# Optimization experiments

Hardware: AMD Instinct MI355X
Metric: run time of the kernel (lower is better)

The kernel has to match this reference:

```python
import jax, jax.numpy as jnp
import numpy as np

B, S, HID = 2, 2048, 1024
H, D = 16, 64
SCALE = D ** -0.5


def setup_inputs() -> dict:
    key = jax.random.key(0)
    ks = jax.random.split(key, 7)
    std = HID ** -0.5
    return {
        "x": jax.random.normal(ks[0], (B, S, HID), jnp.float32),
        "Wq": jax.random.normal(ks[1], (HID, HID), jnp.float32) * std,
        "Wk": jax.random.normal(ks[2], (HID, HID), jnp.float32) * std,
        "Wv": jax.random.normal(ks[3], (HID, HID), jnp.float32) * std,
        "Wf": jax.random.normal(ks[4], (H, HID), jnp.float32) * std,
        "bf": jnp.zeros((H,), jnp.float32),
        "Wo": jax.random.normal(ks[5], (HID, HID), jnp.float32) * std,
    }


def reference(x, Wq, Wk, Wv, Wf, bf, Wo):
    b, s, _ = x.shape
    # projections (torch Linear: y = x @ W.T), reshape to [b, h, s, d]
    q = (x @ Wq.T).reshape(b, s, H, D).transpose(0, 2, 1, 3)
    k = (x @ Wk.T).reshape(b, s, H, D).transpose(0, 2, 1, 3)
    v = (x @ Wv.T).reshape(b, s, H, D).transpose(0, 2, 1, 3)
    # forget gate: [b, h, s]
    f = jax.nn.sigmoid(x @ Wf.T + bf).transpose(0, 2, 1)
    cum_log_f = jnp.cumsum(jnp.log(f + 1e-6), axis=-1)  # [b, h, s]
    # bias[i, j] = cum[i] - cum[j]
    bias = cum_log_f[..., :, None] - cum_log_f[..., None, :]  # [b, h, s, s]
    causal = jnp.tril(jnp.ones((s, s), bool))
    bias = jnp.where(causal, bias, -jnp.inf)
    scores = jnp.einsum("bhid,bhjd->bhij", q, k) * SCALE + bias
    attn = jax.nn.softmax(scores, axis=-1)
    out = jnp.einsum("bhij,bhjd->bhid", attn, v)  # [b, h, s, d]
    out = out.transpose(0, 2, 1, 3).reshape(b, s, H * D)
    return out @ Wo.T
```

## Files before the change

kernel.cpp:

```cpp
#include <hip/hip_runtime.h>
#include <hip/hip_bf16.h>
#include <math.h>

typedef __attribute__((ext_vector_type(8))) short bf16x8;
typedef __attribute__((ext_vector_type(4))) short s16x4;
typedef __attribute__((ext_vector_type(4))) float f32x4;
typedef __attribute__((ext_vector_type(2))) int i32x2;

constexpr int NB = 2, NS = 2048, NHID = 1024, NH = 16, ND = 64;
constexpr float FSCALE = 0.125f;
constexpr float LOG2E  = 1.44269504088896f;
constexpr int QBLK = 128, NT = NS / QBLK;
constexpr float DROP_MARGIN = 30.0f;

__device__ __forceinline__ short f2bf(float f) {
    union { __hip_bfloat16 h; short s; } u;
    u.h = __float2bfloat16(f);
    return u.s;
}

__device__ __forceinline__ float bf2f(short s) {
    union { unsigned u; float f; } u;
    u.u = ((unsigned)(unsigned short)s) << 16;
    return u.f;
}

__device__ __forceinline__ void gload16(const void* g, void* l) {
    __builtin_amdgcn_global_load_lds(
        (const __attribute__((address_space(1))) unsigned*)g,
        (__attribute__((address_space(3))) unsigned*)l, 16, 0, 0);
}

__device__ __forceinline__ unsigned lds_addr(void* p) {
    return (unsigned)(size_t)(__attribute__((address_space(3))) void*)p;
}

__global__ __launch_bounds__(256)
void cast_kernel(const float* __restrict__ x,
                 const float* __restrict__ Wq, const float* __restrict__ Wk,
                 const float* __restrict__ Wv, const float* __restrict__ Wo,
                 short* __restrict__ xb,
                 short* __restrict__ Wqb, short* __restrict__ Wkb,
                 short* __restrict__ Wvb, short* __restrict__ Wob) {
    const int bx = blockIdx.x;
    const float* s; short* d; size_t i;
    if (bx < 2048) {
        s = x; d = xb;
        i = ((size_t)bx*256 + threadIdx.x)*8;
    } else {
        const int widx = (bx - 2048) >> 9, blk = (bx - 2048) & 511;
        switch (widx) {
            case 0:  s = Wq; d = Wqb; break;
            case 1:  s = Wk; d = Wkb; break;
            case 2:  s = Wv; d = Wvb; break;
            default: s = Wo; d = Wob; break;
        }
        i = ((size_t)blk*256 + threadIdx.x)*8;
    }
    float4 a = *(const float4*)(s+i);
    float4 b = *(const float4*)(s+i+4);
    bf16x8 o;
    o[0]=f2bf(a.x); o[1]=f2bf(a.y); o[2]=f2bf(a.z); o[3]=f2bf(a.w);
    o[4]=f2bf(b.x); o[5]=f2bf(b.y); o[6]=f2bf(b.z); o[7]=f2bf(b.w);
    *(bf16x8*)(d+i) = o;
}

__global__ __launch_bounds__(256)
void fgate_kernel(const float* __restrict__ X, const float* __restrict__ Wf,
                  const float* __restrict__ bfb, float* __restrict__ LF) {
    const int lane = threadIdx.x & 63, w = threadIdx.x >> 6;
    const int m = blockIdx.x;
    const int b = m >> 11, s = m & (NS - 1);
    float xv[16];
    #pragma unroll
    for (int c = 0; c < 16; ++c) xv[c] = X[(size_t)m * NHID + c * 64 + lane];
    #pragma unroll
    for (int hh = 0; hh < 4; ++hh) {
        const int h = w * 4 + hh;
        float p = 0.f;
        #pragma unroll
        for (int c = 0; c < 16; ++c)
            p = fmaf(xv[c], Wf[(size_t)h * NHID + c * 64 + lane], p);
        #pragma unroll
        for (int off = 32; off > 0; off >>= 1) p += __shfl_down(p, off);
        if (lane == 0) {
            float z = p + bfb[h];
            float f = 1.f / (1.f + expf(-z));
            LF[(size_t)(b * NH + h) * NS + s] = __log2f(f + 1e-6f);
        }
    }
}

template<int FM, int FN, int MODE>
__device__ __forceinline__ void gemm_body(
    const short* __restrict__ A, const short* __restrict__ Bm,
    float* __restrict__ Cf, short* __restrict__ Cb,
    int N, int K, float mult, int bx, int by, short* As, short* Bs)
{
    constexpr int BM = FM*32, BN = FN*32;
    const int t = threadIdx.x, w = t>>6, l = t&63, g = l>>4, r = l&15;
    const int m0 = by*BM, n0 = bx*BN;
    const int wr = (w>>1)*(FM*16), wc = (w&1)*(FN*16);
    f32x4 acc[FM][FN] = {};
    for (int k0 = 0; k0 < K; k0 += 32) {
        #pragma unroll
        for (int c = 0; c < (BM*4)/256; ++c) {
            int ci = (c*4 + w)*64 + l;
            gload16(A + (size_t)(m0 + (ci>>2))*K + k0 + (ci&3)*8, As + (c*4+w)*512);
        }
        #pragma unroll
        for (int c = 0; c < (BN*4)/256; ++c) {
            int ci = (c*4 + w)*64 + l;
            gload16(Bm + (size_t)(n0 + (ci>>2))*K + k0 + (ci&3)*8, Bs + (c*4+w)*512);
        }
        __syncthreads();
        bf16x8 af[FM], bfv[FN];
        #pragma unroll
        for (int fm = 0; fm < FM; ++fm)
            af[fm] = *(const bf16x8*)(As + (wr + fm*16 + r)*32 + g*8);
        #pragma unroll
        for (int fn = 0; fn < FN; ++fn)
            bfv[fn] = *(const bf16x8*)(Bs + (wc + fn*16 + r)*32 + g*8);
        #pragma unroll
        for (int fm = 0; fm < FM; ++fm)
            #pragma unroll
            for (int fn = 0; fn < FN; ++fn)
                acc[fm][fn] = __builtin_amdgcn_mfma_f32_16x16x32_bf16(
                    af[fm], bfv[fn], acc[fm][fn], 0, 0, 0);
        __syncthreads();
    }
    #pragma unroll
    for (int fm = 0; fm < FM; ++fm)
        #pragma unroll
        for (int fn = 0; fn < FN; ++fn)
            #pragma unroll
            for (int rr = 0; rr < 4; ++rr) {
                int m = m0 + wr + fm*16 + g*4 + rr;
                int n = n0 + wc + fn*16 + r;
                float v = acc[fm][fn][rr] * mult;
                if (MODE == 0) {
                    Cf[(size_t)m*N + n] = v;
                } else {
                    int b = m >> 11, s = m & (NS-1), hh = n >> 6, d = n & (ND-1);
                    Cb[((size_t)(b*NH + hh)*NS + s)*ND + d] = f2bf(v);
                }
            }
}

__global__ __launch_bounds__(256)
void gemm_qkv_kernel(const short* __restrict__ X,
                     const short* __restrict__ Wq, const short* __restrict__ Wk,
                     const short* __restrict__ Wv,
                     short* __restrict__ Q, short* __restrict__ Kd, short* __restrict__ V)
{
    __shared__ short As[128*32], Bs[128*32];
    const int fl = blockIdx.x + 8*blockIdx.y + 256*blockIdx.z;
    const int wk = (fl & 7)*96 + (fl >> 3);
    const int bx = wk & 7, by = (wk >> 3) & 31, bz = wk >> 8;
    const short* Bm; short* Dst; float mult;
    if (bz == 0)      { Bm = Wq; Dst = Q;  mult = FSCALE * LOG2E; }
    else if (bz == 1) { Bm = Wk; Dst = Kd; mult = 1.f; }
    else              { Bm = Wv; Dst = V;  mult = 1.f; }
    gemm_body<4,4,1>(X, Bm, nullptr, Dst, NHID, NHID, mult, bx, by, As, Bs);
}

__global__ __launch_bounds__(256)
void gemm_out_kernel(const short* __restrict__ A, const short* __restrict__ Wo,
                     float* __restrict__ C)
{
    __shared__ short As[64*32], Bs[128*32];
    const int fl = blockIdx.x + 8*blockIdx.y;
    const int wk = (fl & 7)*64 + (fl >> 3);
    const int bx = wk & 7, by = wk >> 3;
    gemm_body<2,4,0>(A, Wo, C, nullptr, NHID, NHID, 1.f, bx, by, As, Bs);
}

__global__ __launch_bounds__(256)
void aux_kernel(const float* __restrict__ LF, float* __restrict__ CUM,
                const short* __restrict__ Kg, float* __restrict__ KNMAX) {
    const int t = threadIdx.x;
    if (blockIdx.x < 32) {
        __shared__ float ps[256];
        const float* src = LF + (size_t)blockIdx.x * NS;
        float* dst       = CUM + (size_t)blockIdx.x * NS;
        float v[8];
        float tot = 0.f;
        #pragma unroll
        for (int i = 0; i < 8; ++i) { v[i] = src[t * 8 + i]; tot += v[i]; v[i] = tot; }
        ps[t] = tot;
        __syncthreads();
        for (int off = 1; off < 256; off <<= 1) {
            float add = (t >= off) ? ps[t - off] : 0.f;
            __syncthreads();
            ps[t] += add;
            __syncthreads();
        }
        float excl = ps[t] - tot;
        #pragma unroll
        for (int i = 0; i < 8; ++i) dst[t * 8 + i] = excl + v[i];
    } else {
        const int bh = blockIdx.x - 32;
        const short* Kb = Kg + (size_t)bh * NS * ND;
        float mx = 0.f;
        for (int rr = 0; rr < NS/256; ++rr) {
            int row = t * (NS/256) + rr;
            float s = 0.f;
            const bf16x8* p = (const bf16x8*)(Kb + (size_t)row * ND);
            #pragma unroll
            for (int c = 0; c < 8; ++c) {
                bf16x8 v = p[c];
                #pragma unroll
                for (int e = 0; e < 8; ++e) { float f = bf2f(v[e]); s = fmaf(f, f, s); }
            }
            mx = fmaxf(mx, s);
        }
        __shared__ float red[256];
        red[t] = mx; __syncthreads();
        for (int o = 128; o > 0; o >>= 1) {
            if (t < o) red[t] = fmaxf(red[t], red[t+o]);
            __syncthreads();
        }
        if (t == 0) KNMAX[bh] = sqrtf(red[0]);
    }
}

__global__ __launch_bounds__(512)
void attn_mfma(const short* __restrict__ Qg, const short* __restrict__ Kg,
               const short* __restrict__ Vg, const float* __restrict__ CUM,
               const float* __restrict__ KNMAX, short* __restrict__ ATT) {
    __shared__ short Ks[2][64*64];
    __shared__ short Vs[2][64*64];
    __shared__ short Ps[8][16*64];
    const int t = threadIdx.x, w = t>>6, l = t&63, g = l>>4, r = l&15;
    const int bh = blockIdx.y, b = bh>>4, h = bh&15;
    const int tile = blockIdx.x;
    const int i0 = tile * QBLK;
    const size_t base = (size_t)bh * NS * ND;
    const float* cumb = CUM + (size_t)bh * NS;
    char* PsB = (char*)Ps[w];
    const int iwm = i0 + w*16;
    const int iw  = iwm + r;

    bf16x8 qf[2];
    qf[0] = *(const bf16x8*)(Qg + base + (size_t)iw*ND + g*8);
    qf[1] = *(const bf16x8*)(Qg + base + (size_t)iw*ND + 32 + g*8);
    float qs = 0.f;
    #pragma unroll
    for (int e = 0; e < 8; ++e) {
        float f0 = bf2f(qf[0][e]); qs = fmaf(f0, f0, qs);
        float f1 = bf2f(qf[1][e]); qs = fmaf(f1, f1, qs);
    }
    qs += __shfl_xor(qs, 16);
    qs += __shfl_xor(qs, 32);
    const float qkb = sqrtf(qs) * KNMAX[bh];

    float mrun = -1e30f, lrun = 0.f;
    f32x4 acc[4] = {};
    const int utop = 2*tile + 1;

    auto STAGE = [&](int jbase, int bufi) {
        const int ci = w*64 + l;
        int row = ci >> 3, col = (ci & 7) * 8;
        int lcol = col ^ ((row & 7) << 3);
        gload16(Kg + base + (size_t)(jbase+row)*ND + lcol, Ks[bufi] + w*512);
        int st = ci >> 3, q8 = ci & 7;
        int jb = st >> 2, db = st & 3, jj = q8 >> 1, dh = q8 & 1;
        gload16(Vg + base + (size_t)(jbase + jb*4 + jj)*ND + db*16 + dh*8,
                Vs[bufi] + w*512);
    };

    STAGE(utop*64, 0);
    __syncthreads();

    #pragma unroll 1
    for (int u = utop; u >= 0; --u) {
        const int cur = (utop - u) & 1;
        const int j0 = u * 64;
        if (u > 0) STAGE((u-1)*64, cur^1);

        const bool live = (j0 <= iwm + 15);
        if (live) {
            const char* KsB = (const char*)Ks[cur];
            const unsigned vsb = lds_addr(Vs[cur]);
            f32x4 sT[4];
            __builtin_amdgcn_s_setprio(1);
            #pragma unroll
            for (int fj = 0; fj < 4; ++fj) {
                int row = fj*16 + r;
                unsigned swz = (unsigned)((row & 7) << 4);
                bf16x8 k0v = *(const bf16x8*)(KsB + ((row*128 +      g*16) ^ swz));
                bf16x8 k1v = *(const bf16x8*)(KsB + ((row*128 + 64 + g*16) ^ swz));
                f32x4 z = {};
                z = __builtin_amdgcn_mfma_f32_16x16x32_bf16(k0v, qf[0], z, 0, 0, 0);
                z = __builtin_amdgcn_mfma_f32_16x16x32_bf16(k1v, qf[1], z, 0, 0, 0);
                sT[fj] = z;
            }
            __builtin_amdgcn_s_setprio(0);

            float p[16];
            const bool pd = (j0 + 63 > iwm);
            #pragma unroll
            for (int fj = 0; fj < 4; ++fj) {
                f32x4 cj = *(const f32x4*)(cumb + j0 + fj*16 + g*4);
                #pragma unroll
                for (int rr = 0; rr < 4; ++rr) {
                    float sv = sT[fj][rr] - cj[rr];
                    if (pd && (j0 + fj*16 + g*4 + rr > iw)) sv = -1e30f;
                    p[fj*4+rr] = sv;
                }
            }
            float m0 = fmaxf(fmaxf(fmaxf(p[0],p[1]), fmaxf(p[2],p[3])),
                             fmaxf(fmaxf(p[4],p[5]), fmaxf(p[6],p[7])));
            float m1 = fmaxf(fmaxf(fmaxf(p[8],p[9]), fmaxf(p[10],p[11])),
                             fmaxf(fmaxf(p[12],p[13]), fmaxf(p[14],p[15])));
            float mx = fmaxf(m0, m1);
            mx = fmaxf(mx, __shfl_xor(mx, 16));
            mx = fmaxf(mx, __shfl_xor(mx, 32));
            float newm = fmaxf(mrun, mx);
            float sc = exp2f(mrun - newm);
            mrun = newm;
            float tsum = 0.f;
            #pragma unroll
            for (int q = 0; q < 16; ++q) { p[q] = exp2f(p[q] - newm); tsum += p[q]; }
            tsum += __shfl_xor(tsum, 16);
            tsum += __shfl_xor(tsum, 32);
            lrun = lrun * sc + tsum;

            {
                unsigned swz = (unsigned)((r & 7) << 4);
                #pragma unroll
                for (int fj = 0; fj < 4; ++fj) {
                    s16x4 pk;
                    pk[0]=f2bf(p[fj*4+0]); pk[1]=f2bf(p[fj*4+1]);
                    pk[2]=f2bf(p[fj*4+2]); pk[3]=f2bf(p[fj*4+3]);
                    *(s16x4*)(PsB + ((r*128 + fj*32 + g*8) ^ swz)) = pk;
                }
            }

            float scr[4];
            #pragma unroll
            for (int rr = 0; rr < 4; ++rr) scr[rr] = __shfl(sc, g*4 + rr);
            #pragma unroll
            for (int fd = 0; fd < 4; ++fd)
                #pragma unroll
                for (int rr = 0; rr < 4; ++rr) acc[fd][rr] *= scr[rr];

            bf16x8 pa[2];
            {
                unsigned swz = (unsigned)((r & 7) << 4);
                pa[0] = *(const bf16x8*)(PsB + ((r*128 +      g*16) ^ swz));
                pa[1] = *(const bf16x8*)(PsB + ((r*128 + 64 + g*16) ^ swz));
            }
            i32x2 vt[4][4];
            #pragma unroll
            for (int fd = 0; fd < 4; ++fd)
                #pragma unroll
                for (int jc = 0; jc < 2; ++jc)
                    #pragma unroll
                    for (int hh = 0; hh < 2; ++hh) {
                        unsigned st = (unsigned)((jc*8 + 2*g + hh)*4 + fd);
                        unsigned ad = vsb + st*128 + (unsigned)r*8;
                        asm volatile("ds_read_b64_tr_b16 %0, %1"
                                     : "=v"(vt[fd][jc*2+hh]) : "v"(ad));
                    }
            asm volatile("s_waitcnt lgkmcnt(0)" ::: "memory");
            __builtin_amdgcn_sched_barrier(0);
            __builtin_amdgcn_s_setprio(1);
            #pragma unroll
            for (int fd = 0; fd < 4; ++fd) {
                union { bf16x8 v; i32x2 d2[2]; } u0, u1;
                u0.d2[0] = vt[fd][0]; u0.d2[1] = vt[fd][1];
                u1.d2[0] = vt[fd][2]; u1.d2[1] = vt[fd][3];
                acc[fd] = __builtin_amdgcn_mfma_f32_16x16x32_bf16(pa[0], u0.v, acc[fd], 0, 0, 0);
                acc[fd] = __builtin_amdgcn_mfma_f32_16x16x32_bf16(pa[1], u1.v, acc[fd], 0, 0, 0);
            }
            __builtin_amdgcn_s_setprio(0);
        }

        if (u > 0) {
            bool d = live ? (qkb - cumb[j0-1] < mrun - DROP_MARGIN) : false;
            asm volatile("s_waitcnt vmcnt(0)" ::: "memory");
            if (__syncthreads_and((int)d)) break;
        }
    }

    float linv[4];
    #pragma unroll
    for (int rr = 0; rr < 4; ++rr) linv[rr] = 1.f / __shfl(lrun, g*4 + rr);
    #pragma unroll
    for (int fd = 0; fd < 4; ++fd)
        #pragma unroll
        for (int rr = 0; rr < 4; ++rr) {
            int i = i0 + w*16 + g*4 + rr;
            ATT[((size_t)(b*NS + i))*NHID + h*ND + fd*16 + r] = f2bf(acc[fd][rr] * linv[rr]);
        }
}

extern "C" void kernel_launch(void* const* d_in, const int* in_sizes, int n_in,
                              void* d_out, int out_size, void* d_ws, size_t ws_size,
                              hipStream_t stream) {
    const float* x  = (const float*)d_in[0];
    const float* Wq = (const float*)d_in[1];
    const float* Wk = (const float*)d_in[2];
    const float* Wv = (const float*)d_in[3];
    const float* Wf = (const float*)d_in[4];
    const float* bf = (const float*)d_in[5];
    const float* Wo = (const float*)d_in[6];
    float* out = (float*)d_out;

    const size_t NTOK = (size_t)NB * NS;
    short* xb  = (short*)d_ws;
    short* Wqb = xb  + NTOK * NHID;
    short* Wkb = Wqb + (size_t)NHID * NHID;
    short* Wvb = Wkb + (size_t)NHID * NHID;
    short* Wob = Wvb + (size_t)NHID * NHID;
    short* Qb  = Wob + (size_t)NHID * NHID;
    short* Kb  = Qb  + NTOK * NHID;
    short* Vb  = Kb  + NTOK * NHID;
    short* ATTb= Vb  + NTOK * NHID;
    float* LF  = (float*)(ATTb + NTOK * NHID);
    float* CUM = LF + (size_t)NB * NH * NS;
    float* KNM = CUM + (size_t)NB * NH * NS;

    cast_kernel<<<4096, 256, 0, stream>>>(x, Wq, Wk, Wv, Wo, xb, Wqb, Wkb, Wvb, Wob);
    fgate_kernel<<<(int)NTOK, 256, 0, stream>>>(x, Wf, bf, LF);
    gemm_qkv_kernel<<<dim3(8, 32, 3), 256, 0, stream>>>(xb, Wqb, Wkb, Wvb, Qb, Kb, Vb);
    aux_kernel<<<64, 256, 0, stream>>>(LF, CUM, Kb, KNM);
    attn_mfma<<<dim3(NT, NB * NH), 512, 0, stream>>>(Qb, Kb, Vb, CUM, KNM, ATTb);
    gemm_out_kernel<<<dim3(8, 64), 256, 0, stream>>>(ATTb, Wob, out);
}
```

Baseline: 103.5 us.

## Replace QKV GEMM with 256x192-tile double-buffered swizzled LDS kernel

Replaces the 128x128-tile QKV projection GEMM with one kernel that treats Wq, Wk and Wv as a single contiguous 3072-row weight and uses 256x192 tiles over 512 threads. It adds a K=64 double-buffered LDS pipeline with XOR-swizzled addressing, explicit vmcnt waits and barriers, and raised wave priority around the MFMA loop. The aim is more data reuse per tile, loads overlapped with compute, and fewer LDS bank conflicts. The cost is a large LDS footprint (about 112 KB) and high register pressure, which limit occupancy. The code also relies on the Q, K, V buffers and the bf16 weights being laid out contiguously.

```diff
diff --git a/kernel.cpp b/kernel.cpp
--- a/kernel.cpp
+++ b/kernel.cpp
@@ -91,11 +91,104 @@
     }
 }
 
-template<int FM, int FN, int MODE>
+__global__ __launch_bounds__(512)
+void gemm_qkv256(const short* __restrict__ X, const short* __restrict__ Wf3,
+                 short* __restrict__ Q3) {
+    __shared__ short As2[2][256*64];
+    __shared__ short Bs2[2][192*64];
+    const int t = threadIdx.x, w = t>>6, l = t&63, g = l>>4, r = l&15;
+    const int wr = w>>2, wc = w&3;
+    const int fl = blockIdx.x;
+    const int wk = (fl & 7)*32 + (fl >> 3);
+    const int by = wk >> 4, bx = wk & 15;
+    const int m0 = by*256, n0 = bx*192;
+    const int K = NHID;
+
+    auto STAGE = [&](int kt) {
+        const int bi = kt & 1;
+        const short* Ab = X  + (size_t)m0*K + kt*64;
+        #pragma unroll
+        for (int a = 0; a < 4; ++a) {
+            int ci = a*512 + t;
+            int row = ci >> 3;
+            int sc8 = ((ci & 7)*8) ^ ((row & 7) << 3);
+            gload16(Ab + (size_t)row*K + sc8, As2[bi] + a*4096 + w*512);
+        }
+        const short* Bb = Wf3 + (size_t)n0*K + kt*64;
+        #pragma unroll
+        for (int a = 0; a < 3; ++a) {
+            int ci = a*512 + t;
+            int row = ci >> 3;
+            int sc8 = ((ci & 7)*8) ^ ((row & 7) << 3);
+            gload16(Bb + (size_t)row*K + sc8, Bs2[bi] + a*4096 + w*512);
+        }
+    };
+
+    f32x4 acc[8][3] = {};
+    STAGE(0);
+    #pragma unroll 1
+    for (int kt = 0; kt < 16; ++kt) {
+        const int cur = kt & 1;
+        if (kt < 15) {
+            STAGE(kt+1);
+            asm volatile("s_waitcnt vmcnt(7)" ::: "memory");
+        } else {
+            asm volatile("s_waitcnt vmcnt(0)" ::: "memory");
+        }
+        __builtin_amdgcn_s_barrier();
+        __builtin_amdgcn_sched_barrier(0);
+        const short* Ac = As2[cur];
+        const short* Bc = Bs2[cur];
+        #pragma unroll
+        for (int ks = 0; ks < 2; ++ks) {
+            bf16x8 af[8], bfr[3];
+            #pragma unroll
+            for (int fm = 0; fm < 8; ++fm) {
+                int row = wr*128 + fm*16 + r;
+                unsigned off = (unsigned)row*64 + (unsigned)((ks*32 + g*8) ^ ((row & 7) << 3));
+                af[fm] = *(const bf16x8*)(Ac + off);
+            }
+            #pragma unroll
+            for (int fn = 0; fn < 3; ++fn) {
+                int row = wc*48 + fn*16 + r;
+                unsigned off = (unsigned)row*64 + (unsigned)((ks*32 + g*8) ^ ((row & 7) << 3));
+                bfr[fn] = *(const bf16x8*)(Bc + off);
+            }
+            __builtin_amdgcn_s_setprio(1);
+            #pragma unroll
+            for (int fm = 0; fm < 8; ++fm)
+                #pragma unroll
+                for (int fn = 0; fn < 3; ++fn)
+                    acc[fm][fn] = __builtin_amdgcn_mfma_f32_16x16x32_bf16(
+                        af[fm], bfr[fn], acc[fm][fn], 0, 0, 0);
+            __builtin_amdgcn_s_setprio(0);
+        }
+        __builtin_amdgcn_s_barrier();
+        __builtin_amdgcn_sched_barrier(0);
+    }
+
+    const float qs = FSCALE * LOG2E;
+    #pragma unroll
+    for (int fm = 0; fm < 8; ++fm)
+        #pragma unroll
+        for (int fn = 0; fn < 3; ++fn)
+            #pragma unroll
+            for (int rr = 0; rr < 4; ++rr) {
+                int m = m0 + wr*128 + fm*16 + g*4 + rr;
+                int n = n0 + wc*48 + fn*16 + r;
+                int mat = n >> 10, nn = n & 1023;
+                int hh = nn >> 6, d = nn & 63;
+                int b = m >> 11, s = m & (NS-1);
+                float v = acc[fm][fn][rr] * (mat == 0 ? qs : 1.f);
+                Q3[(size_t)mat*((size_t)NB*NS*NHID)
+                   + ((size_t)(b*NH + hh)*NS + s)*ND + d] = f2bf(v);
+            }
+}
+
+template<int FM, int FN>
 __device__ __forceinline__ void gemm_body(
     const short* __restrict__ A, const short* __restrict__ Bm,
-    float* __restrict__ Cf, short* __restrict__ Cb,
-    int N, int K, float mult, int bx, int by, short* As, short* Bs)
+    float* __restrict__ Cf, int N, int K, int bx, int by, short* As, short* Bs)
 {
     constexpr int BM = FM*32, BN = FN*32;
     const int t = threadIdx.x, w = t>>6, l = t&63, g = l>>4, r = l&15;
@@ -137,31 +230,8 @@
             for (int rr = 0; rr < 4; ++rr) {
                 int m = m0 + wr + fm*16 + g*4 + rr;
                 int n = n0 + wc + fn*16 + r;
-                float v = acc[fm][fn][rr] * mult;
-                if (MODE == 0) {
-                    Cf[(size_t)m*N + n] = v;
-                } else {
-                    int b = m >> 11, s = m & (NS-1), hh = n >> 6, d = n & (ND-1);
-                    Cb[((size_t)(b*NH + hh)*NS + s)*ND + d] = f2bf(v);
-                }
-            }
-}
-
-__global__ __launch_bounds__(256)
-void gemm_qkv_kernel(const short* __restrict__ X,
-                     const short* __restrict__ Wq, const short* __restrict__ Wk,
-                     const short* __restrict__ Wv,
-                     short* __restrict__ Q, short* __restrict__ Kd, short* __restrict__ V)
-{
-    __shared__ short As[128*32], Bs[128*32];
-    const int fl = blockIdx.x + 8*blockIdx.y + 256*blockIdx.z;
-    const int wk = (fl & 7)*96 + (fl >> 3);
-    const int bx = wk & 7, by = (wk >> 3) & 31, bz = wk >> 8;
-    const short* Bm; short* Dst; float mult;
-    if (bz == 0)      { Bm = Wq; Dst = Q;  mult = FSCALE * LOG2E; }
-    else if (bz == 1) { Bm = Wk; Dst = Kd; mult = 1.f; }
-    else              { Bm = Wv; Dst = V;  mult = 1.f; }
-    gemm_body<4,4,1>(X, Bm, nullptr, Dst, NHID, NHID, mult, bx, by, As, Bs);
+                Cf[(size_t)m*N + n] = acc[fm][fn][rr];
+            }
 }
 
 __global__ __launch_bounds__(256)
@@ -172,7 +242,7 @@
     const int fl = blockIdx.x + 8*blockIdx.y;
     const int wk = (fl & 7)*64 + (fl >> 3);
     const int bx = wk & 7, by = wk >> 3;
-    gemm_body<2,4,0>(A, Wo, C, nullptr, NHID, NHID, 1.f, bx, by, As, Bs);
+    gemm_body<2,4>(A, Wo, C, NHID, NHID, bx, by, As, Bs);
 }
 
 __global__ __launch_bounds__(256)
@@ -424,7 +494,7 @@
 
     cast_kernel<<<4096, 256, 0, stream>>>(x, Wq, Wk, Wv, Wo, xb, Wqb, Wkb, Wvb, Wob);
     fgate_kernel<<<(int)NTOK, 256, 0, stream>>>(x, Wf, bf, LF);
-    gemm_qkv_kernel<<<dim3(8, 32, 3), 256, 0, stream>>>(xb, Wqb, Wkb, Wvb, Qb, Kb, Vb);
+    gemm_qkv256<<<256, 512, 0, stream>>>(xb, Wqb, Qb);
     aux_kernel<<<64, 256, 0, stream>>>(LF, CUM, Kb, KNM);
     attn_mfma<<<dim3(NT, NB * NH), 512, 0, stream>>>(Qb, Kb, Vb, CUM, KNM, ATTb);
     gemm_out_kernel<<<dim3(8, 64), 256, 0, stream>>>(ATTb, Wob, out);
```

After: 105.1 us. About the same (+1.5%).
